# Kernel optimization log

Measured on AMD Instinct MI355X. Metric: run time of the kernel, lower is better.

Reference implementation:

```python
import jax, jax.numpy as jnp
import numpy as np

N_NODES = 50000
N_EDGES = 1_600_000
IN_DIM, HID_DIM, OUT_DIM = 128, 128, 64


def setup_inputs() -> dict:
    key = jax.random.key(0)
    k_x, k_e, k_w1, k_b1, k_w2, k_b2 = jax.random.split(key, 6)
    x = jax.random.normal(k_x, (N_NODES, IN_DIM), dtype=jnp.float32)
    edge_index = jax.random.randint(k_e, (2, N_EDGES), 0, N_NODES)
    # Learned params (PyG GCNConv: linear weight + bias per layer)
    W1 = jax.random.normal(k_w1, (IN_DIM, HID_DIM), dtype=jnp.float32) * (1.0 / np.sqrt(IN_DIM))
    b1 = jax.random.normal(k_b1, (HID_DIM,), dtype=jnp.float32) * 0.02
    W2 = jax.random.normal(k_w2, (HID_DIM, OUT_DIM), dtype=jnp.float32) * (1.0 / np.sqrt(HID_DIM))
    b2 = jax.random.normal(k_b2, (OUT_DIM,), dtype=jnp.float32) * 0.02
    return {"x": x, "edge_index": edge_index, "W1": W1, "b1": b1, "W2": W2, "b2": b2}


def _gcn_conv(x, W, b, src, dst, norm, n):
    # x: [N, d_in]; transform first (d small), then gather-scale-scatter over edges.
    xw = x @ W                                   # [N, d_out]
    msg = xw[src] * norm[:, None]                # [E+N, d_out] gathered messages
    out = jax.ops.segment_sum(msg, dst, num_segments=n)
    return out + b


def reference(x, edge_index, W1, b1, W2, b2):
    n = x.shape[0]
    # GCN normalization with self-loops: A_hat = D^-1/2 (A + I) D^-1/2
    loop = jnp.arange(n, dtype=edge_index.dtype)
    src = jnp.concatenate([edge_index[0], loop])
    dst = jnp.concatenate([edge_index[1], loop])
    deg = jnp.zeros((n,), x.dtype).at[dst].add(1.0)
    dinv = jnp.where(deg > 0, jax.lax.rsqrt(deg), 0.0)
    norm = dinv[src] * dinv[dst]                 # [E+N]
    h = _gcn_conv(x, W1, b1, src, dst, norm, n)
    h = jax.nn.relu(h)
    # F.dropout(training=self.training): eval mode -> identity
    out = _gcn_conv(h, W2, b2, src, dst, norm, n)
    return out
```

## Files before the change

### kernel.cpp

```cpp
#include <hip/hip_runtime.h>
#include <cstddef>

#define MAXB 512
#define BSHIFT 7
#define ACHUNK 8192

__device__ inline unsigned pack_bf16x2(float a, float b) {
    unsigned ua = __float_as_uint(a), ub = __float_as_uint(b);
    ua = (ua + 0x7FFFu + ((ua >> 16) & 1u)) >> 16;
    ub = (ub + 0x7FFFu + ((ub >> 16) & 1u)) >> 16;
    return ua | (ub << 16);
}
__device__ inline float bf_lo(unsigned u) { return __uint_as_float(u << 16); }
__device__ inline float bf_hi(unsigned u) { return __uint_as_float(u & 0xFFFF0000u); }

__global__ __launch_bounds__(512) void k_zero512(int* __restrict__ p) {
    p[threadIdx.x] = 0;
}

__global__ __launch_bounds__(256) void k_histA(const int* __restrict__ dst, int* __restrict__ bcnt,
                                               int E, int nbuck) {
    __shared__ int hist[MAXB];
    const int tid = threadIdx.x;
    const int e0  = blockIdx.x * ACHUNK;
    const int e1  = min(e0 + ACHUNK, E);
    for (int i = tid; i < nbuck; i += 256) hist[i] = 0;
    __syncthreads();
    for (int e = e0 + tid; e < e1; e += 256)
        atomicAdd(&hist[dst[e] >> BSHIFT], 1);
    __syncthreads();
    for (int i = tid; i < nbuck; i += 256)
        if (hist[i]) atomicAdd(&bcnt[i], hist[i]);
}

__global__ __launch_bounds__(512) void k_bscan(const int* __restrict__ bcnt, int* __restrict__ bstart,
                                               int* __restrict__ bcur) {
    __shared__ int sh[512];
    const int t = threadIdx.x;
    int v = bcnt[t];
    sh[t] = v;
    __syncthreads();
    for (int d = 1; d < 512; d <<= 1) {
        int u = (t >= d) ? sh[t - d] : 0;
        __syncthreads();
        sh[t] += u;
        __syncthreads();
    }
    int ex = sh[t] - v;
    bstart[t] = ex;
    bcur[t]   = ex;
}

__global__ __launch_bounds__(256) void k_passA(const int* __restrict__ src, const int* __restrict__ dst,
                                               int* __restrict__ bcur, int2* __restrict__ tmp,
                                               int E, int nbuck) {
    __shared__ int hist[MAXB];
    __shared__ int gbase[MAXB];
    const int tid = threadIdx.x;
    const int e0  = blockIdx.x * ACHUNK;
    const int e1  = min(e0 + ACHUNK, E);
    for (int i = tid; i < nbuck; i += 256) hist[i] = 0;
    __syncthreads();
    for (int e = e0 + tid; e < e1; e += 256)
        atomicAdd(&hist[dst[e] >> BSHIFT], 1);
    __syncthreads();
    for (int i = tid; i < nbuck; i += 256) {
        int c = hist[i];
        gbase[i] = c ? atomicAdd(&bcur[i], c) : 0;
        hist[i] = 0;
    }
    __syncthreads();
    for (int e = e0 + tid; e < e1; e += 256) {
        int d = dst[e];
        int b = d >> BSHIFT;
        int slot = atomicAdd(&hist[b], 1);
        tmp[gbase[b] + slot] = make_int2(src[e], d);
    }
}

__global__ __launch_bounds__(256) void k_passB(const int2* __restrict__ tmp, const int* __restrict__ bstart,
                                               const int* __restrict__ bcnt, int* __restrict__ deg,
                                               float* __restrict__ dinv, int* __restrict__ off,
                                               int* __restrict__ esrc, int N) {
    __shared__ int cnt[1 << BSHIFT];
    __shared__ int loff[1 << BSHIFT];
    __shared__ int cur[1 << BSHIFT];
    const int b     = blockIdx.x;
    const int tid   = threadIdx.x;
    const int node0 = b << BSHIFT;
    const int base  = bstart[b];
    const int cntB  = bcnt[b];

    if (tid < 128) cnt[tid] = 0;
    __syncthreads();
    for (int i = tid; i < cntB; i += 256)
        atomicAdd(&cnt[tmp[base + i].y - node0], 1);
    __syncthreads();
    if (tid < 128) loff[tid] = cnt[tid];
    __syncthreads();
    for (int d = 1; d < 128; d <<= 1) {
        int u = (tid >= d && tid < 128) ? loff[tid - d] : 0;
        __syncthreads();
        if (tid < 128) loff[tid] += u;
        __syncthreads();
    }
    if (tid < 128) {
        int c  = cnt[tid];
        int ex = loff[tid] - c;
        cur[tid] = ex;
        if (node0 + tid < N) {
            deg [node0 + tid] = c + 1;
            dinv[node0 + tid] = rsqrtf((float)(c + 1));
            off [node0 + tid] = base + ex;
        }
    }
    __syncthreads();
    for (int i = tid; i < cntB; i += 256) {
        int2 ent = tmp[base + i];
        int  pos = atomicAdd(&cur[ent.y - node0], 1);
        esrc[base + pos] = ent.x;
    }
}

__global__ __launch_bounds__(256) void k_gemm1(const float* __restrict__ x, const float* __restrict__ W,
                                               unsigned* __restrict__ xwb, int M) {
    __shared__ float ws[128 * 128];
    __shared__ float xs[128][32];
    const int tid  = threadIdx.x;
    const int row0 = blockIdx.x * 32;

    for (int i = tid * 4; i < 128 * 128; i += 1024)
        *(float4*)&ws[i] = *(const float4*)&W[i];

    for (int i = tid; i < 32 * 32; i += 256) {
        int r  = i >> 5;
        int cc = (i & 31) << 2;
        float4 v = make_float4(0.f, 0.f, 0.f, 0.f);
        if (row0 + r < M) v = *(const float4*)&x[(size_t)(row0 + r) * 128 + cc];
        xs[cc + 0][r] = v.x; xs[cc + 1][r] = v.y; xs[cc + 2][r] = v.z; xs[cc + 3][r] = v.w;
    }
    __syncthreads();

    const int c0 = (tid & 31) << 2;
    const int r0 = (tid >> 5) << 2;
    float4 a0 = {0,0,0,0}, a1 = {0,0,0,0}, a2 = {0,0,0,0}, a3 = {0,0,0,0};
#pragma unroll 8
    for (int k = 0; k < 128; ++k) {
        float4 wv = *(const float4*)&ws[k * 128 + c0];
        float4 xv = *(const float4*)&xs[k][r0];
        a0.x += xv.x * wv.x; a0.y += xv.x * wv.y; a0.z += xv.x * wv.z; a0.w += xv.x * wv.w;
        a1.x += xv.y * wv.x; a1.y += xv.y * wv.y; a1.z += xv.y * wv.z; a1.w += xv.y * wv.w;
        a2.x += xv.z * wv.x; a2.y += xv.z * wv.y; a2.z += xv.z * wv.z; a2.w += xv.z * wv.w;
        a3.x += xv.w * wv.x; a3.y += xv.w * wv.y; a3.z += xv.w * wv.z; a3.w += xv.w * wv.w;
    }
    uint2* o = (uint2*)xwb;
    if (row0 + r0 + 0 < M) o[(size_t)(row0 + r0 + 0) * 32 + (c0 >> 2)] = make_uint2(pack_bf16x2(a0.x, a0.y), pack_bf16x2(a0.z, a0.w));
    if (row0 + r0 + 1 < M) o[(size_t)(row0 + r0 + 1) * 32 + (c0 >> 2)] = make_uint2(pack_bf16x2(a1.x, a1.y), pack_bf16x2(a1.z, a1.w));
    if (row0 + r0 + 2 < M) o[(size_t)(row0 + r0 + 2) * 32 + (c0 >> 2)] = make_uint2(pack_bf16x2(a2.x, a2.y), pack_bf16x2(a2.z, a2.w));
    if (row0 + r0 + 3 < M) o[(size_t)(row0 + r0 + 3) * 32 + (c0 >> 2)] = make_uint2(pack_bf16x2(a3.x, a3.y), pack_bf16x2(a3.z, a3.w));
}

__global__ __launch_bounds__(256) void k_gemm2(const float* __restrict__ h_in, const float* __restrict__ W,
                                               unsigned* __restrict__ hwb, int M) {
    __shared__ float ws[128 * 64];
    __shared__ float xs[128][32];
    const int tid  = threadIdx.x;
    const int row0 = blockIdx.x * 32;

    for (int i = tid * 4; i < 128 * 64; i += 1024)
        *(float4*)&ws[i] = *(const float4*)&W[i];

    for (int i = tid; i < 32 * 32; i += 256) {
        int r  = i >> 5;
        int cc = (i & 31) << 2;
        float4 v = make_float4(0.f, 0.f, 0.f, 0.f);
        if (row0 + r < M) {
            v = *(const float4*)&h_in[(size_t)(row0 + r) * 128 + cc];
            v.x = fmaxf(v.x, 0.f); v.y = fmaxf(v.y, 0.f);
            v.z = fmaxf(v.z, 0.f); v.w = fmaxf(v.w, 0.f);
        }
        xs[cc + 0][r] = v.x; xs[cc + 1][r] = v.y; xs[cc + 2][r] = v.z; xs[cc + 3][r] = v.w;
    }
    __syncthreads();

    const int c0 = (tid & 15) << 2;
    const int r0 = (tid >> 4) << 1;
    float4 a0 = {0,0,0,0}, a1 = {0,0,0,0};
#pragma unroll 8
    for (int k = 0; k < 128; ++k) {
        float4 wv = *(const float4*)&ws[k * 64 + c0];
        float2 xv = *(const float2*)&xs[k][r0];
        a0.x += xv.x * wv.x; a0.y += xv.x * wv.y; a0.z += xv.x * wv.z; a0.w += xv.x * wv.w;
        a1.x += xv.y * wv.x; a1.y += xv.y * wv.y; a1.z += xv.y * wv.z; a1.w += xv.y * wv.w;
    }
    uint2* o = (uint2*)hwb;
    if (row0 + r0 + 0 < M) o[(size_t)(row0 + r0 + 0) * 16 + (c0 >> 2)] = make_uint2(pack_bf16x2(a0.x, a0.y), pack_bf16x2(a0.z, a0.w));
    if (row0 + r0 + 1 < M) o[(size_t)(row0 + r0 + 1) * 16 + (c0 >> 2)] = make_uint2(pack_bf16x2(a1.x, a1.y), pack_bf16x2(a1.z, a1.w));
}

__global__ __launch_bounds__(256) void k_agg1(const uint2* __restrict__ xwb, const int* __restrict__ esrc,
                                              const int* __restrict__ off, const int* __restrict__ deg,
                                              const float* __restrict__ dinv, const float* __restrict__ b,
                                              float* __restrict__ out1, int N) {
    const int node = blockIdx.x * 4 + (threadIdx.x >> 6);
    if (node >= N) return;
    const int lane = threadIdx.x & 63;
    const int half = lane >> 5;
    const int lc   = lane & 31;
    const int c0   = lc << 2;

    const float di = dinv[node];
    float4 acc0 = {0,0,0,0}, acc1 = {0,0,0,0}, acc2 = {0,0,0,0}, acc3 = {0,0,0,0};
    if (half == 0) {
        float w0 = di * di;
        uint2  sv = xwb[(size_t)node * 32 + lc];
        float4 bb = *(const float4*)&b[c0];
        acc0.x = bb.x + bf_lo(sv.x) * w0; acc0.y = bb.y + bf_hi(sv.x) * w0;
        acc0.z = bb.z + bf_lo(sv.y) * w0; acc0.w = bb.w + bf_hi(sv.y) * w0;
    }

    const int base = off[node];
    const int cnt  = deg[node] - 1;
    for (int p0 = 0; p0 < cnt; p0 += 64) {
        int   es = 0;
        float ew = 0.f;
        if (p0 + lane < cnt) {
            es = esrc[base + p0 + lane];
            ew = dinv[es] * di;
        }
        const int take = min(64, cnt - p0);
        int j = 0;
        for (; j + 16 <= take; j += 16) {
            int i0 = j + half,      i1 = j + 2 + half,  i2 = j + 4 + half,  i3 = j + 6 + half;
            int i4 = j + 8 + half,  i5 = j + 10 + half, i6 = j + 12 + half, i7 = j + 14 + half;
            int   s0 = __shfl(es, i0); float w0f = __shfl(ew, i0);
            int   s1 = __shfl(es, i1); float w1f = __shfl(ew, i1);
            int   s2 = __shfl(es, i2); float w2f = __shfl(ew, i2);
            int   s3 = __shfl(es, i3); float w3f = __shfl(ew, i3);
            int   s4 = __shfl(es, i4); float w4f = __shfl(ew, i4);
            int   s5 = __shfl(es, i5); float w5f = __shfl(ew, i5);
            int   s6 = __shfl(es, i6); float w6f = __shfl(ew, i6);
            int   s7 = __shfl(es, i7); float w7f = __shfl(ew, i7);
            uint2 v0 = xwb[(size_t)s0 * 32 + lc];
            uint2 v1 = xwb[(size_t)s1 * 32 + lc];
            uint2 v2 = xwb[(size_t)s2 * 32 + lc];
            uint2 v3 = xwb[(size_t)s3 * 32 + lc];
            uint2 v4 = xwb[(size_t)s4 * 32 + lc];
            uint2 v5 = xwb[(size_t)s5 * 32 + lc];
            uint2 v6 = xwb[(size_t)s6 * 32 + lc];
            uint2 v7 = xwb[(size_t)s7 * 32 + lc];
            acc0.x += bf_lo(v0.x) * w0f; acc0.y += bf_hi(v0.x) * w0f;
            acc0.z += bf_lo(v0.y) * w0f; acc0.w += bf_hi(v0.y) * w0f;
            acc1.x += bf_lo(v1.x) * w1f; acc1.y += bf_hi(v1.x) * w1f;
            acc1.z += bf_lo(v1.y) * w1f; acc1.w += bf_hi(v1.y) * w1f;
            acc2.x += bf_lo(v2.x) * w2f; acc2.y += bf_hi(v2.x) * w2f;
            acc2.z += bf_lo(v2.y) * w2f; acc2.w += bf_hi(v2.y) * w2f;
            acc3.x += bf_lo(v3.x) * w3f; acc3.y += bf_hi(v3.x) * w3f;
            acc3.z += bf_lo(v3.y) * w3f; acc3.w += bf_hi(v3.y) * w3f;
            acc0.x += bf_lo(v4.x) * w4f; acc0.y += bf_hi(v4.x) * w4f;
            acc0.z += bf_lo(v4.y) * w4f; acc0.w += bf_hi(v4.y) * w4f;
            acc1.x += bf_lo(v5.x) * w5f; acc1.y += bf_hi(v5.x) * w5f;
            acc1.z += bf_lo(v5.y) * w5f; acc1.w += bf_hi(v5.y) * w5f;
            acc2.x += bf_lo(v6.x) * w6f; acc2.y += bf_hi(v6.x) * w6f;
            acc2.z += bf_lo(v6.y) * w6f; acc2.w += bf_hi(v6.y) * w6f;
            acc3.x += bf_lo(v7.x) * w7f; acc3.y += bf_hi(v7.x) * w7f;
            acc3.z += bf_lo(v7.y) * w7f; acc3.w += bf_hi(v7.y) * w7f;
        }
        for (; j + 8 <= take; j += 8) {
            int i0 = j + half, i1 = j + 2 + half, i2 = j + 4 + half, i3 = j + 6 + half;
            int   s0 = __shfl(es, i0); float w0f = __shfl(ew, i0);
            int   s1 = __shfl(es, i1); float w1f = __shfl(ew, i1);
            int   s2 = __shfl(es, i2); float w2f = __shfl(ew, i2);
            int   s3 = __shfl(es, i3); float w3f = __shfl(ew, i3);
            uint2 v0 = xwb[(size_t)s0 * 32 + lc];
            uint2 v1 = xwb[(size_t)s1 * 32 + lc];
            uint2 v2 = xwb[(size_t)s2 * 32 + lc];
            uint2 v3 = xwb[(size_t)s3 * 32 + lc];
            acc0.x += bf_lo(v0.x) * w0f; acc0.y += bf_hi(v0.x) * w0f;
            acc0.z += bf_lo(v0.y) * w0f; acc0.w += bf_hi(v0.y) * w0f;
            acc1.x += bf_lo(v1.x) * w1f; acc1.y += bf_hi(v1.x) * w1f;
            acc1.z += bf_lo(v1.y) * w1f; acc1.w += bf_hi(v1.y) * w1f;
            acc2.x += bf_lo(v2.x) * w2f; acc2.y += bf_hi(v2.x) * w2f;
            acc2.z += bf_lo(v2.y) * w2f; acc2.w += bf_hi(v2.y) * w2f;
            acc3.x += bf_lo(v3.x) * w3f; acc3.y += bf_hi(v3.x) * w3f;
            acc3.z += bf_lo(v3.y) * w3f; acc3.w += bf_hi(v3.y) * w3f;
        }
        for (; j < take; j += 2) {
            int i0 = j + half;
            int   s0 = __shfl(es, i0); float w0f = __shfl(ew, i0);
            uint2 v0 = xwb[(size_t)s0 * 32 + lc];
            acc0.x += bf_lo(v0.x) * w0f; acc0.y += bf_hi(v0.x) * w0f;
            acc0.z += bf_lo(v0.y) * w0f; acc0.w += bf_hi(v0.y) * w0f;
        }
    }
    acc0.x += acc1.x + acc2.x + acc3.x;
    acc0.y += acc1.y + acc2.y + acc3.y;
    acc0.z += acc1.z + acc2.z + acc3.z;
    acc0.w += acc1.w + acc2.w + acc3.w;
    acc0.x += __shfl_xor(acc0.x, 32);
    acc0.y += __shfl_xor(acc0.y, 32);
    acc0.z += __shfl_xor(acc0.z, 32);
    acc0.w += __shfl_xor(acc0.w, 32);
    if (half == 0) *(float4*)&out1[(size_t)node * 128 + c0] = acc0;
}

__global__ __launch_bounds__(256) void k_agg2(const uint2* __restrict__ hwb, const int* __restrict__ esrc,
                                              const int* __restrict__ off, const int* __restrict__ deg,
                                              const float* __restrict__ dinv, const float* __restrict__ b,
                                              float* __restrict__ out, int N) {
    const int node = blockIdx.x * 4 + (threadIdx.x >> 6);
    if (node >= N) return;
    const int lane = threadIdx.x & 63;
    const int grp  = lane >> 4;
    const int lc   = lane & 15;
    const int c0   = lc << 2;

    const float di = dinv[node];
    float4 acc0 = {0,0,0,0}, acc1 = {0,0,0,0}, acc2 = {0,0,0,0}, acc3 = {0,0,0,0};
    if (grp == 0) {
        float w0 = di * di;
        uint2  sv = hwb[(size_t)node * 16 + lc];
        float4 bb = *(const float4*)&b[c0];
        acc0.x = bb.x + bf_lo(sv.x) * w0; acc0.y = bb.y + bf_hi(sv.x) * w0;
        acc0.z = bb.z + bf_lo(sv.y) * w0; acc0.w = bb.w + bf_hi(sv.y) * w0;
    }

    const int base = off[node];
    const int cnt  = deg[node] - 1;
    for (int p0 = 0; p0 < cnt; p0 += 64) {
        int   es = 0;
        float ew = 0.f;
        if (p0 + lane < cnt) {
            es = esrc[base + p0 + lane];
            ew = dinv[es] * di;
        }
        const int take = min(64, cnt - p0);
        int j = 0;
        for (; j + 32 <= take; j += 32) {
            int i0 = j + grp,      i1 = j + 4 + grp,  i2 = j + 8 + grp,  i3 = j + 12 + grp;
            int i4 = j + 16 + grp, i5 = j + 20 + grp, i6 = j + 24 + grp, i7 = j + 28 + grp;
            int   s0 = __shfl(es, i0); float w0f = __shfl(ew, i0);
            int   s1 = __shfl(es, i1); float w1f = __shfl(ew, i1);
            int   s2 = __shfl(es, i2); float w2f = __shfl(ew, i2);
            int   s3 = __shfl(es, i3); float w3f = __shfl(ew, i3);
            int   s4 = __shfl(es, i4); float w4f = __shfl(ew, i4);
            int   s5 = __shfl(es, i5); float w5f = __shfl(ew, i5);
            int   s6 = __shfl(es, i6); float w6f = __shfl(ew, i6);
            int   s7 = __shfl(es, i7); float w7f = __shfl(ew, i7);
            uint2 v0 = hwb[(size_t)s0 * 16 + lc];
            uint2 v1 = hwb[(size_t)s1 * 16 + lc];
            uint2 v2 = hwb[(size_t)s2 * 16 + lc];
            uint2 v3 = hwb[(size_t)s3 * 16 + lc];
            uint2 v4 = hwb[(size_t)s4 * 16 + lc];
            uint2 v5 = hwb[(size_t)s5 * 16 + lc];
            uint2 v6 = hwb[(size_t)s6 * 16 + lc];
            uint2 v7 = hwb[(size_t)s7 * 16 + lc];
            acc0.x += bf_lo(v0.x) * w0f; acc0.y += bf_hi(v0.x) * w0f;
            acc0.z += bf_lo(v0.y) * w0f; acc0.w += bf_hi(v0.y) * w0f;
            acc1.x += bf_lo(v1.x) * w1f; acc1.y += bf_hi(v1.x) * w1f;
            acc1.z += bf_lo(v1.y) * w1f; acc1.w += bf_hi(v1.y) * w1f;
            acc2.x += bf_lo(v2.x) * w2f; acc2.y += bf_hi(v2.x) * w2f;
            acc2.z += bf_lo(v2.y) * w2f; acc2.w += bf_hi(v2.y) * w2f;
            acc3.x += bf_lo(v3.x) * w3f; acc3.y += bf_hi(v3.x) * w3f;
            acc3.z += bf_lo(v3.y) * w3f; acc3.w += bf_hi(v3.y) * w3f;
            acc0.x += bf_lo(v4.x) * w4f; acc0.y += bf_hi(v4.x) * w4f;
            acc0.z += bf_lo(v4.y) * w4f; acc0.w += bf_hi(v4.y) * w4f;
            acc1.x += bf_lo(v5.x) * w5f; acc1.y += bf_hi(v5.x) * w5f;
            acc1.z += bf_lo(v5.y) * w5f; acc1.w += bf_hi(v5.y) * w5f;
            acc2.x += bf_lo(v6.x) * w6f; acc2.y += bf_hi(v6.x) * w6f;
            acc2.z += bf_lo(v6.y) * w6f; acc2.w += bf_hi(v6.y) * w6f;
            acc3.x += bf_lo(v7.x) * w7f; acc3.y += bf_hi(v7.x) * w7f;
            acc3.z += bf_lo(v7.y) * w7f; acc3.w += bf_hi(v7.y) * w7f;
        }
        for (; j + 16 <= take; j += 16) {
            int i0 = j + grp, i1 = j + 4 + grp, i2 = j + 8 + grp, i3 = j + 12 + grp;
            int   s0 = __shfl(es, i0); float w0f = __shfl(ew, i0);
            int   s1 = __shfl(es, i1); float w1f = __shfl(ew, i1);
            int   s2 = __shfl(es, i2); float w2f = __shfl(ew, i2);
            int   s3 = __shfl(es, i3); float w3f = __shfl(ew, i3);
            uint2 v0 = hwb[(size_t)s0 * 16 + lc];
            uint2 v1 = hwb[(size_t)s1 * 16 + lc];
            uint2 v2 = hwb[(size_t)s2 * 16 + lc];
            uint2 v3 = hwb[(size_t)s3 * 16 + lc];
            acc0.x += bf_lo(v0.x) * w0f; acc0.y += bf_hi(v0.x) * w0f;
            acc0.z += bf_lo(v0.y) * w0f; acc0.w += bf_hi(v0.y) * w0f;
            acc1.x += bf_lo(v1.x) * w1f; acc1.y += bf_hi(v1.x) * w1f;
            acc1.z += bf_lo(v1.y) * w1f; acc1.w += bf_hi(v1.y) * w1f;
            acc2.x += bf_lo(v2.x) * w2f; acc2.y += bf_hi(v2.x) * w2f;
            acc2.z += bf_lo(v2.y) * w2f; acc2.w += bf_hi(v2.y) * w2f;
            acc3.x += bf_lo(v3.x) * w3f; acc3.y += bf_hi(v3.x) * w3f;
            acc3.z += bf_lo(v3.y) * w3f; acc3.w += bf_hi(v3.y) * w3f;
        }
        for (; j < take; j += 4) {
            int i0 = j + grp;
            int   s0 = __shfl(es, i0); float w0f = __shfl(ew, i0);
            uint2 v0 = hwb[(size_t)s0 * 16 + lc];
            acc0.x += bf_lo(v0.x) * w0f; acc0.y += bf_hi(v0.x) * w0f;
            acc0.z += bf_lo(v0.y) * w0f; acc0.w += bf_hi(v0.y) * w0f;
        }
    }
    acc0.x += acc1.x + acc2.x + acc3.x;
    acc0.y += acc1.y + acc2.y + acc3.y;
    acc0.z += acc1.z + acc2.z + acc3.z;
    acc0.w += acc1.w + acc2.w + acc3.w;
    acc0.x += __shfl_xor(acc0.x, 16); acc0.y += __shfl_xor(acc0.y, 16);
    acc0.z += __shfl_xor(acc0.z, 16); acc0.w += __shfl_xor(acc0.w, 16);
    acc0.x += __shfl_xor(acc0.x, 32); acc0.y += __shfl_xor(acc0.y, 32);
    acc0.z += __shfl_xor(acc0.z, 32); acc0.w += __shfl_xor(acc0.w, 32);
    if (lane < 16) *(float4*)&out[(size_t)node * 64 + c0] = acc0;
}

extern "C" void kernel_launch(void* const* d_in, const int* in_sizes, int n_in,
                              void* d_out, int out_size, void* d_ws, size_t ws_size,
                              hipStream_t stream) {
    const float* x  = (const float*)d_in[0];
    const int*   ei = (const int*)  d_in[1];
    const float* W1 = (const float*)d_in[2];
    const float* b1 = (const float*)d_in[3];
    const float* W2 = (const float*)d_in[4];
    const float* b2 = (const float*)d_in[5];
    float* out = (float*)d_out;

    const int N = in_sizes[0] / 128;
    const int E = in_sizes[1] / 2;
    const int* src = ei;
    const int* dst = ei + E;
    const int NBUCK = (N + 127) / 128;
    const int NA    = (E + ACHUNK - 1) / ACHUNK;

    char* w = (char*)d_ws;
    int*      deg     = (int*)w;              w += (size_t)N * 4;
    float*    dinv    = (float*)w;            w += (size_t)N * 4;
    int*      off     = (int*)w;              w += (size_t)N * 4;
    int*      bstart  = (int*)w;              w += 512 * 4;
    int*      bcnt    = (int*)w;              w += 512 * 4;
    int*      bcur    = (int*)w;              w += 512 * 4;
    int*      esrc    = (int*)w;              w += (size_t)E * 4;
    unsigned* xwb     = (unsigned*)w;         w += (size_t)N * 128 * 2;
    float*    out1    = (float*)w;            w += (size_t)N * 128 * 4;
    unsigned* hwb     = (unsigned*)w;
    int2*     tmp     = (int2*)out1;

    k_zero512 <<<1, 512, 0, stream>>>(bcnt);
    k_histA   <<<NA, 256, 0, stream>>>(dst, bcnt, E, NBUCK);
    k_bscan   <<<1, 512, 0, stream>>>(bcnt, bstart, bcur);
    k_passA   <<<NA, 256, 0, stream>>>(src, dst, bcur, tmp, E, NBUCK);
    k_passB   <<<NBUCK, 256, 0, stream>>>(tmp, bstart, bcnt, deg, dinv, off, esrc, N);

    k_gemm1 <<<(N + 31) / 32, 256, 0, stream>>>(x, W1, xwb, N);
    k_agg1  <<<(N + 3) / 4, 256, 0, stream>>>((const uint2*)xwb, esrc, off, deg, dinv, b1, out1, N);

    k_gemm2 <<<(N + 31) / 32, 256, 0, stream>>>(out1, W2, hwb, N);
    k_agg2  <<<(N + 3) / 4, 256, 0, stream>>>((const uint2*)hwb, esrc, off, deg, dinv, b2, out, N);
}
```

Baseline: 252.1 us.

## Use bf16 MFMA for both dense transforms and nontemporal hints in aggregation

Both GEMM kernels are rewritten to convert inputs and weights to bf16 and use 16x16x32 bf16 MFMA instructions, with a transposed padded weight tile in shared memory and output staged through LDS for coalesced stores. Tiles grow to 64 rows per block. The aggregation kernels also switch edge-index loads and output stores to nontemporal hints to reduce cache pollution. Inputs are now rounded to bf16 before the multiply, which adds precision loss on the activations.

```diff
diff --git a/kernel.cpp b/kernel.cpp
--- a/kernel.cpp
+++ b/kernel.cpp
@@ -4,6 +4,9 @@
 #define MAXB 512
 #define BSHIFT 7
 #define ACHUNK 8192
+
+typedef __attribute__((ext_vector_type(8))) short short8;
+typedef __attribute__((ext_vector_type(4))) float f32x4;
 
 __device__ inline unsigned pack_bf16x2(float a, float b) {
     unsigned ua = __float_as_uint(a), ub = __float_as_uint(b);
@@ -11,8 +14,17 @@
     ub = (ub + 0x7FFFu + ((ub >> 16) & 1u)) >> 16;
     return ua | (ub << 16);
 }
+__device__ inline unsigned short bf16rne(float f) {
+    unsigned u = __float_as_uint(f);
+    return (unsigned short)((u + 0x7FFFu + ((u >> 16) & 1u)) >> 16);
+}
 __device__ inline float bf_lo(unsigned u) { return __uint_as_float(u << 16); }
 __device__ inline float bf_hi(unsigned u) { return __uint_as_float(u & 0xFFFF0000u); }
+
+__device__ inline void nt_store4(const float4& v, float* p) {
+    f32x4 t = { v.x, v.y, v.z, v.w };
+    __builtin_nontemporal_store(t, (f32x4*)p);
+}
 
 __global__ __launch_bounds__(512) void k_zero512(int* __restrict__ p) {
     p[threadIdx.x] = 0;
@@ -123,79 +135,115 @@
 }
 
 __global__ __launch_bounds__(256) void k_gemm1(const float* __restrict__ x, const float* __restrict__ W,
-                                               unsigned* __restrict__ xwb, int M) {
-    __shared__ float ws[128 * 128];
-    __shared__ float xs[128][32];
+                                               unsigned short* __restrict__ xwb, int M) {
+    __shared__ unsigned short Wt[128 * 144];
+    __shared__ unsigned short outS[64 * 128];
     const int tid  = threadIdx.x;
-    const int row0 = blockIdx.x * 32;
-
-    for (int i = tid * 4; i < 128 * 128; i += 1024)
-        *(float4*)&ws[i] = *(const float4*)&W[i];
-
-    for (int i = tid; i < 32 * 32; i += 256) {
-        int r  = i >> 5;
-        int cc = (i & 31) << 2;
-        float4 v = make_float4(0.f, 0.f, 0.f, 0.f);
-        if (row0 + r < M) v = *(const float4*)&x[(size_t)(row0 + r) * 128 + cc];
-        xs[cc + 0][r] = v.x; xs[cc + 1][r] = v.y; xs[cc + 2][r] = v.z; xs[cc + 3][r] = v.w;
-    }
-    __syncthreads();
-
-    const int c0 = (tid & 31) << 2;
-    const int r0 = (tid >> 5) << 2;
-    float4 a0 = {0,0,0,0}, a1 = {0,0,0,0}, a2 = {0,0,0,0}, a3 = {0,0,0,0};
-#pragma unroll 8
-    for (int k = 0; k < 128; ++k) {
-        float4 wv = *(const float4*)&ws[k * 128 + c0];
-        float4 xv = *(const float4*)&xs[k][r0];
-        a0.x += xv.x * wv.x; a0.y += xv.x * wv.y; a0.z += xv.x * wv.z; a0.w += xv.x * wv.w;
-        a1.x += xv.y * wv.x; a1.y += xv.y * wv.y; a1.z += xv.y * wv.z; a1.w += xv.y * wv.w;
-        a2.x += xv.z * wv.x; a2.y += xv.z * wv.y; a2.z += xv.z * wv.z; a2.w += xv.z * wv.w;
-        a3.x += xv.w * wv.x; a3.y += xv.w * wv.y; a3.z += xv.w * wv.z; a3.w += xv.w * wv.w;
-    }
-    uint2* o = (uint2*)xwb;
-    if (row0 + r0 + 0 < M) o[(size_t)(row0 + r0 + 0) * 32 + (c0 >> 2)] = make_uint2(pack_bf16x2(a0.x, a0.y), pack_bf16x2(a0.z, a0.w));
-    if (row0 + r0 + 1 < M) o[(size_t)(row0 + r0 + 1) * 32 + (c0 >> 2)] = make_uint2(pack_bf16x2(a1.x, a1.y), pack_bf16x2(a1.z, a1.w));
-    if (row0 + r0 + 2 < M) o[(size_t)(row0 + r0 + 2) * 32 + (c0 >> 2)] = make_uint2(pack_bf16x2(a2.x, a2.y), pack_bf16x2(a2.z, a2.w));
-    if (row0 + r0 + 3 < M) o[(size_t)(row0 + r0 + 3) * 32 + (c0 >> 2)] = make_uint2(pack_bf16x2(a3.x, a3.y), pack_bf16x2(a3.z, a3.w));
+    const int row0 = blockIdx.x * 64;
+
+    for (int i = tid; i < 128 * 128; i += 256) {
+        int k = i >> 7, col = i & 127;
+        Wt[col * 144 + k] = bf16rne(W[i]);
+    }
+    __syncthreads();
+
+    const int w  = tid >> 6, l = tid & 63;
+    const int lr = l & 15,  kg = l >> 4;
+    const int row = row0 + w * 16 + lr;
+
+    f32x4 zero4 = {0.f, 0.f, 0.f, 0.f};
+    f32x4 acc[8];
+#pragma unroll
+    for (int ct = 0; ct < 8; ++ct) acc[ct] = zero4;
+
+#pragma unroll
+    for (int ks = 0; ks < 4; ++ks) {
+        uint4 aw = make_uint4(0u, 0u, 0u, 0u);
+        if (row < M) {
+            const float* ap = x + (size_t)row * 128 + ks * 32 + kg * 8;
+            float4 u = *(const float4*)ap;
+            float4 v = *(const float4*)(ap + 4);
+            aw = make_uint4(pack_bf16x2(u.x, u.y), pack_bf16x2(u.z, u.w),
+                            pack_bf16x2(v.x, v.y), pack_bf16x2(v.z, v.w));
+        }
+        short8 afrag = *(short8*)&aw;
+#pragma unroll
+        for (int ct = 0; ct < 8; ++ct) {
+            short8 bfrag = *(const short8*)&Wt[(ct * 16 + lr) * 144 + ks * 32 + kg * 8];
+            acc[ct] = __builtin_amdgcn_mfma_f32_16x16x32_bf16(afrag, bfrag, acc[ct], 0, 0, 0);
+        }
+    }
+
+#pragma unroll
+    for (int ct = 0; ct < 8; ++ct)
+#pragma unroll
+        for (int q = 0; q < 4; ++q)
+            outS[(w * 16 + kg * 4 + q) * 128 + ct * 16 + lr] = bf16rne(acc[ct][q]);
+    __syncthreads();
+
+    for (int i = 0; i < 4; ++i) {
+        int idx = i * 256 + tid;
+        int r   = idx >> 4;
+        if (row0 + r < M)
+            ((uint4*)xwb)[(size_t)row0 * 16 + idx] = ((const uint4*)outS)[idx];
+    }
 }
 
 __global__ __launch_bounds__(256) void k_gemm2(const float* __restrict__ h_in, const float* __restrict__ W,
-                                               unsigned* __restrict__ hwb, int M) {
-    __shared__ float ws[128 * 64];
-    __shared__ float xs[128][32];
+                                               unsigned short* __restrict__ hwb, int M) {
+    __shared__ unsigned short Wt[64 * 144];
+    __shared__ unsigned short outS[64 * 64];
     const int tid  = threadIdx.x;
-    const int row0 = blockIdx.x * 32;
-
-    for (int i = tid * 4; i < 128 * 64; i += 1024)
-        *(float4*)&ws[i] = *(const float4*)&W[i];
-
-    for (int i = tid; i < 32 * 32; i += 256) {
-        int r  = i >> 5;
-        int cc = (i & 31) << 2;
-        float4 v = make_float4(0.f, 0.f, 0.f, 0.f);
-        if (row0 + r < M) {
-            v = *(const float4*)&h_in[(size_t)(row0 + r) * 128 + cc];
-            v.x = fmaxf(v.x, 0.f); v.y = fmaxf(v.y, 0.f);
-            v.z = fmaxf(v.z, 0.f); v.w = fmaxf(v.w, 0.f);
-        }
-        xs[cc + 0][r] = v.x; xs[cc + 1][r] = v.y; xs[cc + 2][r] = v.z; xs[cc + 3][r] = v.w;
-    }
-    __syncthreads();
-
-    const int c0 = (tid & 15) << 2;
-    const int r0 = (tid >> 4) << 1;
-    float4 a0 = {0,0,0,0}, a1 = {0,0,0,0};
-#pragma unroll 8
-    for (int k = 0; k < 128; ++k) {
-        float4 wv = *(const float4*)&ws[k * 64 + c0];
-        float2 xv = *(const float2*)&xs[k][r0];
-        a0.x += xv.x * wv.x; a0.y += xv.x * wv.y; a0.z += xv.x * wv.z; a0.w += xv.x * wv.w;
-        a1.x += xv.y * wv.x; a1.y += xv.y * wv.y; a1.z += xv.y * wv.z; a1.w += xv.y * wv.w;
-    }
-    uint2* o = (uint2*)hwb;
-    if (row0 + r0 + 0 < M) o[(size_t)(row0 + r0 + 0) * 16 + (c0 >> 2)] = make_uint2(pack_bf16x2(a0.x, a0.y), pack_bf16x2(a0.z, a0.w));
-    if (row0 + r0 + 1 < M) o[(size_t)(row0 + r0 + 1) * 16 + (c0 >> 2)] = make_uint2(pack_bf16x2(a1.x, a1.y), pack_bf16x2(a1.z, a1.w));
+    const int row0 = blockIdx.x * 64;
+
+    for (int i = tid; i < 128 * 64; i += 256) {
+        int k = i >> 6, col = i & 63;
+        Wt[col * 144 + k] = bf16rne(W[i]);
+    }
+    __syncthreads();
+
+    const int w  = tid >> 6, l = tid & 63;
+    const int lr = l & 15,  kg = l >> 4;
+    const int row = row0 + w * 16 + lr;
+
+    f32x4 zero4 = {0.f, 0.f, 0.f, 0.f};
+    f32x4 acc[4];
+#pragma unroll
+    for (int ct = 0; ct < 4; ++ct) acc[ct] = zero4;
+
+#pragma unroll
+    for (int ks = 0; ks < 4; ++ks) {
+        uint4 aw = make_uint4(0u, 0u, 0u, 0u);
+        if (row < M) {
+            const float* ap = h_in + (size_t)row * 128 + ks * 32 + kg * 8;
+            float4 u = *(const float4*)ap;
+            float4 v = *(const float4*)(ap + 4);
+            u.x = fmaxf(u.x, 0.f); u.y = fmaxf(u.y, 0.f); u.z = fmaxf(u.z, 0.f); u.w = fmaxf(u.w, 0.f);
+            v.x = fmaxf(v.x, 0.f); v.y = fmaxf(v.y, 0.f); v.z = fmaxf(v.z, 0.f); v.w = fmaxf(v.w, 0.f);
+            aw = make_uint4(pack_bf16x2(u.x, u.y), pack_bf16x2(u.z, u.w),
+                            pack_bf16x2(v.x, v.y), pack_bf16x2(v.z, v.w));
+        }
+        short8 afrag = *(short8*)&aw;
+#pragma unroll
+        for (int ct = 0; ct < 4; ++ct) {
+            short8 bfrag = *(const short8*)&Wt[(ct * 16 + lr) * 144 + ks * 32 + kg * 8];
+            acc[ct] = __builtin_amdgcn_mfma_f32_16x16x32_bf16(afrag, bfrag, acc[ct], 0, 0, 0);
+        }
+    }
+
+#pragma unroll
+    for (int ct = 0; ct < 4; ++ct)
+#pragma unroll
+        for (int q = 0; q < 4; ++q)
+            outS[(w * 16 + kg * 4 + q) * 64 + ct * 16 + lr] = bf16rne(acc[ct][q]);
+    __syncthreads();
+
+    for (int i = 0; i < 2; ++i) {
+        int idx = i * 256 + tid;
+        int r   = idx >> 3;
+        if (row0 + r < M)
+            ((uint4*)hwb)[(size_t)row0 * 8 + idx] = ((const uint4*)outS)[idx];
+    }
 }
 
 __global__ __launch_bounds__(256) void k_agg1(const uint2* __restrict__ xwb, const int* __restrict__ esrc,
@@ -225,7 +273,7 @@
         int   es = 0;
         float ew = 0.f;
         if (p0 + lane < cnt) {
-            es = esrc[base + p0 + lane];
+            es = __builtin_nontemporal_load(&esrc[base + p0 + lane]);
             ew = dinv[es] * di;
         }
         const int take = min(64, cnt - p0);
@@ -301,7 +349,8 @@
     acc0.y += __shfl_xor(acc0.y, 32);
     acc0.z += __shfl_xor(acc0.z, 32);
     acc0.w += __shfl_xor(acc0.w, 32);
-    if (half == 0) *(float4*)&out1[(size_t)node * 128 + c0] = acc0;
+    if (half == 0)
+        nt_store4(acc0, &out1[(size_t)node * 128 + c0]);
 }
 
 __global__ __launch_bounds__(256) void k_agg2(const uint2* __restrict__ hwb, const int* __restrict__ esrc,
@@ -331,7 +380,7 @@
         int   es = 0;
         float ew = 0.f;
         if (p0 + lane < cnt) {
-            es = esrc[base + p0 + lane];
+            es = __builtin_nontemporal_load(&esrc[base + p0 + lane]);
             ew = dinv[es] * di;
         }
         const int take = min(64, cnt - p0);
@@ -407,7 +456,8 @@
     acc0.z += __shfl_xor(acc0.z, 16); acc0.w += __shfl_xor(acc0.w, 16);
     acc0.x += __shfl_xor(acc0.x, 32); acc0.y += __shfl_xor(acc0.y, 32);
     acc0.z += __shfl_xor(acc0.z, 32); acc0.w += __shfl_xor(acc0.w, 32);
-    if (lane < 16) *(float4*)&out[(size_t)node * 64 + c0] = acc0;
+    if (lane < 16)
+        nt_store4(acc0, &out[(size_t)node * 64 + c0]);
 }
 
 extern "C" void kernel_launch(void* const* d_in, const int* in_sizes, int n_in,
@@ -427,19 +477,20 @@
     const int* dst = ei + E;
     const int NBUCK = (N + 127) / 128;
     const int NA    = (E + ACHUNK - 1) / ACHUNK;
+    const int NG    = (N + 63) / 64;
 
     char* w = (char*)d_ws;
-    int*      deg     = (int*)w;              w += (size_t)N * 4;
-    float*    dinv    = (float*)w;            w += (size_t)N * 4;
-    int*      off     = (int*)w;              w += (size_t)N * 4;
-    int*      bstart  = (int*)w;              w += 512 * 4;
-    int*      bcnt    = (int*)w;              w += 512 * 4;
-    int*      bcur    = (int*)w;              w += 512 * 4;
-    int*      esrc    = (int*)w;              w += (size_t)E * 4;
-    unsigned* xwb     = (unsigned*)w;         w += (size_t)N * 128 * 2;
-    float*    out1    = (float*)w;            w += (size_t)N * 128 * 4;
-    unsigned* hwb     = (unsigned*)w;
-    int2*     tmp     = (int2*)out1;
+    int*            deg     = (int*)w;        w += (size_t)N * 4;
+    float*          dinv    = (float*)w;      w += (size_t)N * 4;
+    int*            off     = (int*)w;        w += (size_t)N * 4;
+    int*            bstart  = (int*)w;        w += 512 * 4;
+    int*            bcnt    = (int*)w;        w += 512 * 4;
+    int*            bcur    = (int*)w;        w += 512 * 4;
+    int*            esrc    = (int*)w;        w += (size_t)E * 4;
+    unsigned short* xwb     = (unsigned short*)w;  w += (size_t)N * 128 * 2;
+    float*          out1    = (float*)w;      w += (size_t)N * 128 * 4;
+    unsigned short* hwb     = (unsigned short*)w;
+    int2*           tmp     = (int2*)out1;
 
     k_zero512 <<<1, 512, 0, stream>>>(bcnt);
     k_histA   <<<NA, 256, 0, stream>>>(dst, bcnt, E, NBUCK);
@@ -447,9 +498,9 @@
     k_passA   <<<NA, 256, 0, stream>>>(src, dst, bcur, tmp, E, NBUCK);
     k_passB   <<<NBUCK, 256, 0, stream>>>(tmp, bstart, bcnt, deg, dinv, off, esrc, N);
 
-    k_gemm1 <<<(N + 31) / 32, 256, 0, stream>>>(x, W1, xwb, N);
+    k_gemm1 <<<NG, 256, 0, stream>>>(x, W1, xwb, N);
     k_agg1  <<<(N + 3) / 4, 256, 0, stream>>>((const uint2*)xwb, esrc, off, deg, dinv, b1, out1, N);
 
-    k_gemm2 <<<(N + 31) / 32, 256, 0, stream>>>(out1, W2, hwb, N);
+    k_gemm2 <<<NG, 256, 0, stream>>>(out1, W2, hwb, N);
     k_agg2  <<<(N + 3) / 4, 256, 0, stream>>>((const uint2*)hwb, esrc, off, deg, dinv, b2, out, N);
 }
```

Measured after the change: 209.7 us. 1.2x faster.
